# Kernel tuning notes

Hardware: AMD Instinct MI355X
Metric: run time of the kernel (lower is better)

The kernel has to match this reference:

```python
import jax, jax.numpy as jnp
import numpy as np

D_MODEL = 1024
N_HEADS = 16
HEAD_DIM = D_MODEL // N_HEADS  # 64
N_T = max(1, int(N_HEADS * 0.25))  # 4 time heads
N_S = N_HEADS - N_T               # 12 space heads
T_DIM = N_T * HEAD_DIM
S_DIM = N_S * HEAD_DIM
B, L = 2, 2048


def setup_inputs() -> dict:
    key = jax.random.key(0)
    ks = jax.random.split(key, 8)
    std = 0.02
    return {
        "x": jax.random.normal(ks[0], (B, L, D_MODEL), dtype=jnp.float32),
        "attention_mask": jnp.zeros((B, 1, 1, L), dtype=jnp.float32),
        # torch nn.Linear weights have shape (out_features, in_features)
        "w_qt": jax.random.normal(ks[1], (T_DIM, D_MODEL), dtype=jnp.float32) * std,
        "w_kt": jax.random.normal(ks[2], (T_DIM, D_MODEL), dtype=jnp.float32) * std,
        "w_qs": jax.random.normal(ks[3], (S_DIM, D_MODEL), dtype=jnp.float32) * std,
        "w_ks": jax.random.normal(ks[4], (S_DIM, D_MODEL), dtype=jnp.float32) * std,
        "w_sigma": jnp.zeros((1,), dtype=jnp.float32),
        "w_v": jax.random.normal(ks[5], (D_MODEL, D_MODEL), dtype=jnp.float32) * std,
        "w_o": jax.random.normal(ks[6], (D_MODEL, D_MODEL), dtype=jnp.float32) * std,
    }


def _heads(x, w, n_h):
    # x:(B,L,D) @ w.T:(D,out) -> (B,L,n_h,d_h) -> (B,n_h,L,d_h)
    b, l, _ = x.shape
    y = jnp.einsum('bld,td->blt', x, w)
    return y.reshape(b, l, n_h, HEAD_DIM).transpose(0, 2, 1, 3)


def reference(x, attention_mask, w_qt, w_kt, w_qs, w_ks, w_sigma, w_v, w_o):
    b, l, _ = x.shape
    scale = np.sqrt(HEAD_DIM).astype(np.float32)
    # F3: time heads (sign-flipped, scaled by learnable sigma) + space heads
    Qt = _heads(x, w_qt, N_T)
    Kt = _heads(x, w_kt, N_T)
    Qs = _heads(x, w_qs, N_S)
    Ks = _heads(x, w_ks, N_S)
    st = jnp.einsum('bhqd,bhkd->bhqk', Qt, Kt)  # (B,N_T,L,L)
    ss = jnp.einsum('bhqd,bhkd->bhqk', Qs, Ks)  # (B,N_S,L,L)
    sigma = jax.nn.sigmoid(w_sigma[0])
    score = jnp.concatenate([-sigma * st, ss], axis=1) / scale  # (B,H,L,L)
    score = score + attention_mask.astype(score.dtype)
    attn_probs = jax.nn.softmax(score, axis=-1).astype(x.dtype)
    # dropout p=0.0 -> identity
    V = _heads(x, w_v, N_HEADS)  # (B,H,L,d_h)
    out = jnp.einsum('bhqk,bhkd->bhqd', attn_probs, V)
    out = out.transpose(0, 2, 1, 3).reshape(b, l, D_MODEL)
    out = jnp.einsum('bld,od->blo', out, w_o)
    return out, attn_probs
```

## Files before the change

### kernel.cpp

```cpp
#include <hip/hip_runtime.h>

typedef __bf16 bf16x8 __attribute__((ext_vector_type(8)));
typedef float f32x4 __attribute__((ext_vector_type(4)));
typedef float f32x16 __attribute__((ext_vector_type(16)));
typedef short short4v __attribute__((ext_vector_type(4)));
typedef unsigned short ushort8 __attribute__((ext_vector_type(8)));
typedef unsigned int uint4v __attribute__((ext_vector_type(4)));

#define AS1 __attribute__((address_space(1)))
#define AS3 __attribute__((address_space(3)))
#define GLL16(g, l) __builtin_amdgcn_global_load_lds((const AS1 void*)(g), (AS3 void*)(l), 16, 0, 0)
#define MFMA16(a, b, c) __builtin_amdgcn_mfma_f32_16x16x32_bf16((a), (b), (c), 0, 0, 0)
#define MFMA32(a, b, c) __builtin_amdgcn_mfma_f32_32x32x16_bf16((a), (b), (c), 0, 0, 0)
#define WAITVM(N) asm volatile("s_waitcnt vmcnt(" #N ")" ::: "memory")
#define WAITLGKM0 asm volatile("s_waitcnt lgkmcnt(0)" ::: "memory")
#define L2E 1.44269504f

__device__ __forceinline__ unsigned short f2bf(float f) {
  unsigned int u = __builtin_bit_cast(unsigned int, f);
  u = (u + 0x7fffu + ((u >> 16) & 1u)) >> 16;
  return (unsigned short)u;
}

__device__ __forceinline__ unsigned int cvtpk_bf16(float lo, float hi) {
  unsigned int r;
  asm("v_cvt_pk_bf16_f32 %0, %1, %2" : "=v"(r) : "v"(lo), "v"(hi));
  return r;
}

__global__ void convert_kernel(const float* __restrict__ x,
                               const float* __restrict__ w_qt, const float* __restrict__ w_kt,
                               const float* __restrict__ w_qs, const float* __restrict__ w_ks,
                               const float* __restrict__ w_v, const float* __restrict__ w_o,
                               unsigned short* __restrict__ xb, unsigned short* __restrict__ wcat,
                               unsigned short* __restrict__ wob) {
  const int NX = 4096 * 1024, NW = 3072 * 1024, NO = 1024 * 1024;
  int stride = gridDim.x * blockDim.x;
  for (int i = blockIdx.x * blockDim.x + threadIdx.x; i < NX + NW + NO; i += stride) {
    if (i < NX) {
      xb[i] = f2bf(x[i]);
    } else if (i < NX + NW) {
      int j = i - NX;
      int n = j >> 10, k = j & 1023;
      const float* src;
      if (n < 256)        src = w_qt + n * 1024;
      else if (n < 1024)  src = w_qs + (n - 256) * 1024;
      else if (n < 1280)  src = w_kt + (n - 1024) * 1024;
      else if (n < 2048)  src = w_ks + (n - 1280) * 1024;
      else                src = w_v + (n - 2048) * 1024;
      wcat[j] = f2bf(src[k]);
    } else {
      int j = i - NX - NW;
      wob[j] = f2bf(w_o[j]);
    }
  }
}

__global__ __launch_bounds__(256) void gemm_qkv(const unsigned short* __restrict__ A,
                                                const unsigned short* __restrict__ Bw,
                                                const float* __restrict__ amask,
                                                unsigned short* __restrict__ qb,
                                                unsigned short* __restrict__ kb,
                                                unsigned short* __restrict__ vt) {
  __shared__ unsigned short As[128 * 32];
  __shared__ unsigned short Bs[128 * 32];
  const int t = threadIdx.x;
  const int lane = t & 63, wid = t >> 6;
  const int wm = wid >> 1, wn = wid & 1;
  const int lr = lane & 15, lg = lane >> 4;
  const int m0 = blockIdx.x * 128, n0 = blockIdx.y * 128;
  const int K = 1024;
  f32x4 acc[4][4] = {};
  const unsigned short* gA0 = A + (m0 + (t >> 2)) * K + (t & 3) * 8;
  const unsigned short* gB0 = Bw + (n0 + (t >> 2)) * K + (t & 3) * 8;
  char* lA = (char*)As + wid * 1024;
  char* lB = (char*)Bs + wid * 1024;
  for (int k0 = 0; k0 < K; k0 += 32) {
    __syncthreads();
    GLL16(gA0 + k0, lA);
    GLL16(gA0 + 64 * K + k0, lA + 4096);
    GLL16(gB0 + k0, lB);
    GLL16(gB0 + 64 * K + k0, lB + 4096);
    __syncthreads();
    bf16x8 af[4], bfr[4];
#pragma unroll
    for (int i = 0; i < 4; ++i) {
      af[i] = *(const bf16x8*)&As[(wm * 64 + i * 16 + lr) * 32 + lg * 8];
      bfr[i] = *(const bf16x8*)&Bs[(wn * 64 + i * 16 + lr) * 32 + lg * 8];
    }
#pragma unroll
    for (int i = 0; i < 4; ++i)
#pragma unroll
      for (int j = 0; j < 4; ++j)
        acc[i][j] = MFMA16(af[i], bfr[j], acc[i][j]);
  }
#pragma unroll
  for (int i = 0; i < 4; ++i) {
#pragma unroll
    for (int j = 0; j < 4; ++j) {
      int n = n0 + wn * 64 + j * 16 + lr;
      int mb = m0 + wm * 64 + i * 16 + lg * 4;
      f32x4 v = acc[i][j];
      if (n < 2048) {
        unsigned short* dst = (n < 1024) ? qb : kb;
        int nn = n & 1023;
        int h = nn >> 6, d = nn & 63;
#pragma unroll
        for (int r = 0; r < 4; ++r) {
          int m = mb + r;
          int b = m >> 11, l = m & 2047;
          dst[((b * 16 + h) * 2048 + l) * 64 + d] = f2bf(v[r]);
        }
      } else {
        int nn = n - 2048;
        int h = nn >> 6, d = nn & 63;
        int b = mb >> 11, l = mb & 2047;
        const float* mrow = amask + b * 2048 + l;
        short4v pk;
#pragma unroll
        for (int r = 0; r < 4; ++r)
          pk[r] = (short)f2bf(v[r] * __expf(mrow[r]));
        *(short4v*)&vt[((b * 16 + h) * 64 + d) * 2048 + l] = pk;
      }
    }
  }
}

__global__ __launch_bounds__(256, 3) void attn_kernel(const unsigned short* __restrict__ qb,
                                                      const unsigned short* __restrict__ kb,
                                                      const unsigned short* __restrict__ vt,
                                                      const float* __restrict__ mask,
                                                      const float* __restrict__ w_sigma,
                                                      float* __restrict__ probs,
                                                      unsigned short* __restrict__ ao) {
  __shared__ __align__(16) char smem[33408];
  const int t = threadIdx.x;
  const int lane = t & 63, w = t >> 6;
  const int col = lane & 31, hi = lane >> 5;
  const int srow = lane >> 3;
  const int schunk = (lane & 7) ^ (srow & 7);
  const int s = blockIdx.x;
  const int bh = (s & 7) * 4 + ((s >> 3) >> 6);
  const int q0 = ((s >> 3) & 63) * 32;
  const int b = bh >> 4, h = bh & 15;
  const float sigma = 1.0f / (1.0f + __expf(-w_sigma[0]));
  const float fac2 = ((h < 4) ? (-sigma * 0.125f) : 0.125f) * L2E;
  const float* maskb = mask + b * 2048;
  const int kbase = w * 512;

  char* Kl = smem + w * 4096;
  char* Vl = smem + 16384 + w * 4096;
  float (*psum)[32] = (float(*)[32])(smem + 32768);
  float* rsum = (float*)(smem + 33280);
  float* pvacc = (float*)smem;

  const unsigned short* kb_bh = kb + (size_t)bh * 2048 * 64;
  const unsigned short* vt_bh = vt + (size_t)bh * 64 * 2048;

  bf16x8 qf[4];
  {
    const unsigned short* qp = qb + (size_t)(bh * 2048 + q0 + col) * 64 + hi * 8;
#pragma unroll
    for (int m = 0; m < 4; ++m) qf[m] = *(const bf16x8*)(qp + m * 16);
  }

#pragma unroll
  for (int j = 0; j < 4; ++j)
    GLL16(kb_bh + (size_t)(kbase + j * 8 + srow) * 64 + schunk * 8, Kl + j * 1024);
  float rs[16];
#pragma unroll
  for (int r = 0; r < 16; ++r) rs[r] = 0.f;
  for (int c = 0; c < 16; ++c) {
    int kc = kbase + c * 32;
    char* curb = (c & 1) ? Vl : Kl;
    char* nxtb = (c & 1) ? Kl : Vl;
    if (c < 15) {
#pragma unroll
      for (int j = 0; j < 4; ++j)
        GLL16(kb_bh + (size_t)(kc + 32 + j * 8 + srow) * 64 + schunk * 8, nxtb + j * 1024);
      WAITVM(4);
    } else {
      WAITVM(0);
    }
    f32x16 sacc = {};
#pragma unroll
    for (int m = 0; m < 4; ++m) {
      bf16x8 kf = *(const bf16x8*)(curb + col * 128 + (((2 * m + hi) ^ (col & 7)) << 4));
      sacc = MFMA32(qf[m], kf, sacc);
    }
    float mv2 = maskb[kc + col] * L2E;
#pragma unroll
    for (int r = 0; r < 16; ++r) rs[r] += exp2f(sacc[r] * fac2 + mv2);
  }
  WAITLGKM0;
#pragma unroll
  for (int j = 0; j < 4; ++j)
    GLL16(kb_bh + (size_t)(kbase + j * 8 + srow) * 64 + schunk * 8, Kl + j * 1024);
#pragma unroll
  for (int j = 0; j < 4; ++j)
    GLL16(vt_bh + (size_t)(j * 8 + srow + (schunk >> 2) * 32) * 2048 + kbase + (schunk & 3) * 8,
          Vl + j * 1024);
#pragma unroll
  for (int o = 1; o < 32; o <<= 1)
#pragma unroll
    for (int r = 0; r < 16; ++r) rs[r] += __shfl_xor(rs[r], o);
  if (col == 0) {
#pragma unroll
    for (int r = 0; r < 16; ++r) psum[w][(r & 3) + 8 * (r >> 2) + 4 * hi] = rs[r];
  }
  __syncthreads();
  if (t < 32) rsum[t] = -log2f(psum[0][t] + psum[1][t] + psum[2][t] + psum[3][t]);
  __syncthreads();

  float rws_l[16];
#pragma unroll
  for (int r = 0; r < 16; ++r) rws_l[r] = rsum[(r & 3) + 8 * (r >> 2) + 4 * hi];
  const float rws_t = rsum[col];

  f32x16 oacc0 = {}, oacc1 = {};
  float* pp = probs + (size_t)(bh * 2048 + q0) * 2048;
  for (int c = 0; c < 16; ++c) {
    int kc = kbase + c * 32;
    if (c == 0) { WAITVM(4); } else { WAITVM(20); }
    bf16x8 kf[4];
#pragma unroll
    for (int m = 0; m < 4; ++m)
      kf[m] = *(const bf16x8*)(Kl + col * 128 + (((2 * m + hi) ^ (col & 7)) << 4));
    f32x16 sn = {}, st_ = {};
#pragma unroll
    for (int m = 0; m < 4; ++m) {
      sn  = MFMA32(qf[m], kf[m], sn);
      st_ = MFMA32(kf[m], qf[m], st_);
    }
    WAITLGKM0;
    if (c < 15) {
#pragma unroll
      for (int j = 0; j < 4; ++j)
        GLL16(kb_bh + (size_t)(kc + 32 + j * 8 + srow) * 64 + schunk * 8, Kl + j * 1024);
    }
    float mv2 = maskb[kc + col] * L2E;
    float pn[16];
#pragma unroll
    for (int r = 0; r < 16; ++r) pn[r] = exp2f(sn[r] * fac2 + (rws_l[r] + mv2));
    float pt[16];
#pragma unroll
    for (int r = 0; r < 16; ++r) pt[r] = exp2f(fminf(st_[r] * fac2 + rws_t, 60.0f));
    unsigned int A0 = cvtpk_bf16(pt[0], pt[1]),  B0 = cvtpk_bf16(pt[4], pt[5]);
    unsigned int C0 = cvtpk_bf16(pt[2], pt[3]),  D0 = cvtpk_bf16(pt[6], pt[7]);
    unsigned int E0 = cvtpk_bf16(pt[8], pt[9]),  F0 = cvtpk_bf16(pt[12], pt[13]);
    unsigned int G0 = cvtpk_bf16(pt[10], pt[11]), H0 = cvtpk_bf16(pt[14], pt[15]);
    asm("v_permlane32_swap_b32 %0, %1" : "+v"(A0), "+v"(B0));
    asm("v_permlane32_swap_b32 %0, %1" : "+v"(C0), "+v"(D0));
    asm("v_permlane32_swap_b32 %0, %1" : "+v"(E0), "+v"(F0));
    asm("v_permlane32_swap_b32 %0, %1" : "+v"(G0), "+v"(H0));
    uint4v u1; u1[0] = A0; u1[1] = C0; u1[2] = B0; u1[3] = D0;
    uint4v u2; u2[0] = E0; u2[1] = G0; u2[2] = F0; u2[3] = H0;
    bf16x8 frag1 = __builtin_bit_cast(bf16x8, u1);
    bf16x8 frag2 = __builtin_bit_cast(bf16x8, u2);
    if (c == 0) { WAITVM(4); } else if (c < 15) { WAITVM(20); } else { WAITVM(16); }
#pragma unroll
    for (int kh = 0; kh < 2; ++kh) {
      bf16x8 pa = (kh == 0) ? frag1 : frag2;
#pragma unroll
      for (int dh = 0; dh < 2; ++dh) {
        bf16x8 vf = *(const bf16x8*)(Vl + col * 128 + (((dh * 4 + kh * 2 + hi) ^ (col & 7)) << 4));
        if (dh == 0) oacc0 = MFMA32(pa, vf, oacc0);
        else         oacc1 = MFMA32(pa, vf, oacc1);
      }
    }
    WAITLGKM0;
    if (c < 15) {
#pragma unroll
      for (int j = 0; j < 4; ++j)
        GLL16(vt_bh + (size_t)(j * 8 + srow + (schunk >> 2) * 32) * 2048 + kc + 32 + (schunk & 3) * 8,
              Vl + j * 1024);
    }
    float* pr = pp + kc + col;
#pragma unroll
    for (int r = 0; r < 16; ++r) {
      int row = (r & 3) + 8 * (r >> 2) + 4 * hi;
      __builtin_nontemporal_store(pn[r], pr + (size_t)row * 2048);
    }
  }

  __syncthreads();
  for (int i = t; i < 2048; i += 256) pvacc[i] = 0.0f;
  __syncthreads();
#pragma unroll
  for (int r = 0; r < 16; ++r) {
    int row = (r & 3) + 8 * (r >> 2) + 4 * hi;
    atomicAdd(&pvacc[row * 64 + col], oacc0[r]);
    atomicAdd(&pvacc[row * 64 + 32 + col], oacc1[r]);
  }
  __syncthreads();
  {
    int row = t >> 3, c8 = (t & 7) * 8;
    f32x4 v0 = *(const f32x4*)&pvacc[row * 64 + c8];
    f32x4 v1 = *(const f32x4*)&pvacc[row * 64 + c8 + 4];
    ushort8 o;
#pragma unroll
    for (int i = 0; i < 4; ++i) {
      o[i] = f2bf(v0[i]);
      o[i + 4] = f2bf(v1[i]);
    }
    *(ushort8*)&ao[((b * 2048) + q0 + row) * 1024 + h * 64 + c8] = o;
  }
}

__global__ __launch_bounds__(256) void gemm_oproj(const unsigned short* __restrict__ A,
                                                  const unsigned short* __restrict__ Bw,
                                                  float* __restrict__ out) {
  __shared__ unsigned short As[128 * 32];
  __shared__ unsigned short Bs[128 * 32];
  const int t = threadIdx.x;
  const int lane = t & 63, wid = t >> 6;
  const int wm = wid >> 1, wn = wid & 1;
  const int lr = lane & 15, lg = lane >> 4;
  const int m0 = blockIdx.x * 128, n0 = blockIdx.y * 128;
  const int K = 1024;
  f32x4 acc[4][4] = {};
  const unsigned short* gA0 = A + (m0 + (t >> 2)) * K + (t & 3) * 8;
  const unsigned short* gB0 = Bw + (n0 + (t >> 2)) * K + (t & 3) * 8;
  char* lA = (char*)As + wid * 1024;
  char* lB = (char*)Bs + wid * 1024;
  for (int k0 = 0; k0 < K; k0 += 32) {
    __syncthreads();
    GLL16(gA0 + k0, lA);
    GLL16(gA0 + 64 * K + k0, lA + 4096);
    GLL16(gB0 + k0, lB);
    GLL16(gB0 + 64 * K + k0, lB + 4096);
    __syncthreads();
    bf16x8 af[4], bfr[4];
#pragma unroll
    for (int i = 0; i < 4; ++i) {
      af[i] = *(const bf16x8*)&As[(wm * 64 + i * 16 + lr) * 32 + lg * 8];
      bfr[i] = *(const bf16x8*)&Bs[(wn * 64 + i * 16 + lr) * 32 + lg * 8];
    }
#pragma unroll
    for (int i = 0; i < 4; ++i)
#pragma unroll
      for (int j = 0; j < 4; ++j)
        acc[i][j] = MFMA16(af[i], bfr[j], acc[i][j]);
  }
#pragma unroll
  for (int i = 0; i < 4; ++i) {
#pragma unroll
    for (int j = 0; j < 4; ++j) {
      int n = n0 + wn * 64 + j * 16 + lr;
      int mb = m0 + wm * 64 + i * 16 + lg * 4;
#pragma unroll
      for (int r = 0; r < 4; ++r)
        out[(mb + r) * 1024 + n] = acc[i][j][r];
    }
  }
}

extern "C" void kernel_launch(void* const* d_in, const int* in_sizes, int n_in,
                              void* d_out, int out_size, void* d_ws, size_t ws_size,
                              hipStream_t stream) {
  const float* x       = (const float*)d_in[0];
  const float* amask   = (const float*)d_in[1];
  const float* w_qt    = (const float*)d_in[2];
  const float* w_kt    = (const float*)d_in[3];
  const float* w_qs    = (const float*)d_in[4];
  const float* w_ks    = (const float*)d_in[5];
  const float* w_sigma = (const float*)d_in[6];
  const float* w_v     = (const float*)d_in[7];
  const float* w_o     = (const float*)d_in[8];

  char* ws = (char*)d_ws;
  unsigned short* xb   = (unsigned short*)ws;
  unsigned short* wcat = (unsigned short*)(ws + 8388608);
  unsigned short* wob  = (unsigned short*)(ws + 14680064);
  unsigned short* qb   = (unsigned short*)(ws + 16777216);
  unsigned short* kb   = (unsigned short*)(ws + 25165824);
  unsigned short* vt   = (unsigned short*)(ws + 33554432);
  unsigned short* ao   = (unsigned short*)(ws + 41943040);

  float* outp = (float*)d_out;
  float* probs = outp + 4194304;

  convert_kernel<<<2048, 256, 0, stream>>>(x, w_qt, w_kt, w_qs, w_ks, w_v, w_o, xb, wcat, wob);
  gemm_qkv<<<dim3(32, 24), 256, 0, stream>>>(xb, wcat, amask, qb, kb, vt);
  attn_kernel<<<2048, 256, 0, stream>>>(qb, kb, vt, amask, w_sigma, probs, ao);
  gemm_oproj<<<dim3(32, 8), 256, 0, stream>>>(ao, wob, outp);
}
```

Before: 337.2 us.

## Store K and V in MFMA fragment order and load directly to registers

The QKV GEMM epilogue now writes K and V into a pre-swizzled layout that matches the 32x32x16 MFMA operand fragments, one 512-element block per fragment. The attention kernel then loads these fragments straight from global memory into registers with coalesced 16-byte loads. This drops the LDS staging, the async global-to-LDS double buffering and the manual waitcnt handling. In exchange it gives up explicit prefetch overlap and relies on the compiler and cache for latency hiding. The GEMM epilogue also does scattered 2-byte stores for K.

```diff
diff --git a/kernel.cpp b/kernel.cpp
--- a/kernel.cpp
+++ b/kernel.cpp
@@ -12,8 +12,6 @@
 #define GLL16(g, l) __builtin_amdgcn_global_load_lds((const AS1 void*)(g), (AS3 void*)(l), 16, 0, 0)
 #define MFMA16(a, b, c) __builtin_amdgcn_mfma_f32_16x16x32_bf16((a), (b), (c), 0, 0, 0)
 #define MFMA32(a, b, c) __builtin_amdgcn_mfma_f32_32x32x16_bf16((a), (b), (c), 0, 0, 0)
-#define WAITVM(N) asm volatile("s_waitcnt vmcnt(" #N ")" ::: "memory")
-#define WAITLGKM0 asm volatile("s_waitcnt lgkmcnt(0)" ::: "memory")
 #define L2E 1.44269504f
 
 __device__ __forceinline__ unsigned short f2bf(float f) {
@@ -60,8 +58,8 @@
                                                 const unsigned short* __restrict__ Bw,
                                                 const float* __restrict__ amask,
                                                 unsigned short* __restrict__ qb,
-                                                unsigned short* __restrict__ kb,
-                                                unsigned short* __restrict__ vt) {
+                                                unsigned short* __restrict__ kfrag,
+                                                unsigned short* __restrict__ vfrag) {
   __shared__ unsigned short As[128 * 32];
   __shared__ unsigned short Bs[128 * 32];
   const int t = threadIdx.x;
@@ -100,45 +98,57 @@
     for (int j = 0; j < 4; ++j) {
       int n = n0 + wn * 64 + j * 16 + lr;
       int mb = m0 + wm * 64 + i * 16 + lg * 4;
+      int b = mb >> 11, l = mb & 2047;
+      int cg = l >> 5;
       f32x4 v = acc[i][j];
-      if (n < 2048) {
-        unsigned short* dst = (n < 1024) ? qb : kb;
-        int nn = n & 1023;
+      if (n < 1024) {
+        int h = n >> 6, d = n & 63;
+#pragma unroll
+        for (int r = 0; r < 4; ++r)
+          qb[((b * 16 + h) * 2048 + l + r) * 64 + d] = f2bf(v[r]);
+      } else if (n < 2048) {
+        int nn = n - 1024;
         int h = nn >> 6, d = nn & 63;
+        int mfr = d >> 4, hi2 = (d >> 3) & 1, e = d & 7;
 #pragma unroll
         for (int r = 0; r < 4; ++r) {
-          int m = mb + r;
-          int b = m >> 11, l = m & 2047;
-          dst[((b * 16 + h) * 2048 + l) * 64 + d] = f2bf(v[r]);
+          int lr2 = l + r;
+          int cgr = lr2 >> 5, ck = lr2 & 31;
+          size_t idx = ((size_t)((b * 16 + h) * 64 + cgr) * 4 + mfr) * 512 + (hi2 * 32 + ck) * 8 + e;
+          kfrag[idx] = f2bf(v[r]);
         }
       } else {
         int nn = n - 2048;
         int h = nn >> 6, d = nn & 63;
-        int b = mb >> 11, l = mb & 2047;
+        int dh = d >> 5, dcol = d & 31;
+        int kk = l & 31;
+        int kh = kk >> 4, hi2 = (kk >> 3) & 1, i0 = kk & 7;
         const float* mrow = amask + b * 2048 + l;
+        size_t idx = ((size_t)((b * 16 + h) * 64 + (l >> 5)) * 4 + (kh * 2 + dh)) * 512
+                     + (hi2 * 32 + dcol) * 8 + i0;
         short4v pk;
 #pragma unroll
         for (int r = 0; r < 4; ++r)
           pk[r] = (short)f2bf(v[r] * __expf(mrow[r]));
-        *(short4v*)&vt[((b * 16 + h) * 64 + d) * 2048 + l] = pk;
+        *(short4v*)&vfrag[idx] = pk;
       }
     }
   }
 }
 
 __global__ __launch_bounds__(256, 3) void attn_kernel(const unsigned short* __restrict__ qb,
-                                                      const unsigned short* __restrict__ kb,
-                                                      const unsigned short* __restrict__ vt,
+                                                      const unsigned short* __restrict__ kfrag,
+                                                      const unsigned short* __restrict__ vfrag,
                                                       const float* __restrict__ mask,
                                                       const float* __restrict__ w_sigma,
                                                       float* __restrict__ probs,
                                                       unsigned short* __restrict__ ao) {
-  __shared__ __align__(16) char smem[33408];
+  __shared__ __align__(16) float pvacc[2048];
+  __shared__ float psum[4][32];
+  __shared__ float rsum[32];
   const int t = threadIdx.x;
   const int lane = t & 63, w = t >> 6;
   const int col = lane & 31, hi = lane >> 5;
-  const int srow = lane >> 3;
-  const int schunk = (lane & 7) ^ (srow & 7);
   const int s = blockIdx.x;
   const int bh = (s & 7) * 4 + ((s >> 3) >> 6);
   const int q0 = ((s >> 3) & 63) * 32;
@@ -146,16 +156,12 @@
   const float sigma = 1.0f / (1.0f + __expf(-w_sigma[0]));
   const float fac2 = ((h < 4) ? (-sigma * 0.125f) : 0.125f) * L2E;
   const float* maskb = mask + b * 2048;
-  const int kbase = w * 512;
-
-  char* Kl = smem + w * 4096;
-  char* Vl = smem + 16384 + w * 4096;
-  float (*psum)[32] = (float(*)[32])(smem + 32768);
-  float* rsum = (float*)(smem + 33280);
-  float* pvacc = (float*)smem;
-
-  const unsigned short* kb_bh = kb + (size_t)bh * 2048 * 64;
-  const unsigned short* vt_bh = vt + (size_t)bh * 64 * 2048;
+  const int cg0 = w * 16;
+
+  const unsigned short* kfb = kfrag + (size_t)bh * 131072;
+  const unsigned short* vfb = vfrag + (size_t)bh * 131072;
+
+  for (int i = t; i < 2048; i += 256) pvacc[i] = 0.0f;
 
   bf16x8 qf[4];
   {
@@ -164,42 +170,25 @@
     for (int m = 0; m < 4; ++m) qf[m] = *(const bf16x8*)(qp + m * 16);
   }
 
-#pragma unroll
-  for (int j = 0; j < 4; ++j)
-    GLL16(kb_bh + (size_t)(kbase + j * 8 + srow) * 64 + schunk * 8, Kl + j * 1024);
   float rs[16];
 #pragma unroll
   for (int r = 0; r < 16; ++r) rs[r] = 0.f;
   for (int c = 0; c < 16; ++c) {
-    int kc = kbase + c * 32;
-    char* curb = (c & 1) ? Vl : Kl;
-    char* nxtb = (c & 1) ? Kl : Vl;
-    if (c < 15) {
-#pragma unroll
-      for (int j = 0; j < 4; ++j)
-        GLL16(kb_bh + (size_t)(kc + 32 + j * 8 + srow) * 64 + schunk * 8, nxtb + j * 1024);
-      WAITVM(4);
-    } else {
-      WAITVM(0);
-    }
+    int cg = cg0 + c;
+    const unsigned short* kp = kfb + (size_t)cg * 2048 + lane * 8;
+    bf16x8 kf0 = *(const bf16x8*)(kp);
+    bf16x8 kf1 = *(const bf16x8*)(kp + 512);
+    bf16x8 kf2 = *(const bf16x8*)(kp + 1024);
+    bf16x8 kf3 = *(const bf16x8*)(kp + 1536);
+    float mv2 = maskb[cg * 32 + col] * L2E;
     f32x16 sacc = {};
-#pragma unroll
-    for (int m = 0; m < 4; ++m) {
-      bf16x8 kf = *(const bf16x8*)(curb + col * 128 + (((2 * m + hi) ^ (col & 7)) << 4));
-      sacc = MFMA32(qf[m], kf, sacc);
-    }
-    float mv2 = maskb[kc + col] * L2E;
+    sacc = MFMA32(qf[0], kf0, sacc);
+    sacc = MFMA32(qf[1], kf1, sacc);
+    sacc = MFMA32(qf[2], kf2, sacc);
+    sacc = MFMA32(qf[3], kf3, sacc);
 #pragma unroll
     for (int r = 0; r < 16; ++r) rs[r] += exp2f(sacc[r] * fac2 + mv2);
   }
-  WAITLGKM0;
-#pragma unroll
-  for (int j = 0; j < 4; ++j)
-    GLL16(kb_bh + (size_t)(kbase + j * 8 + srow) * 64 + schunk * 8, Kl + j * 1024);
-#pragma unroll
-  for (int j = 0; j < 4; ++j)
-    GLL16(vt_bh + (size_t)(j * 8 + srow + (schunk >> 2) * 32) * 2048 + kbase + (schunk & 3) * 8,
-          Vl + j * 1024);
 #pragma unroll
   for (int o = 1; o < 32; o <<= 1)
 #pragma unroll
@@ -220,34 +209,32 @@
   f32x16 oacc0 = {}, oacc1 = {};
   float* pp = probs + (size_t)(bh * 2048 + q0) * 2048;
   for (int c = 0; c < 16; ++c) {
-    int kc = kbase + c * 32;
-    if (c == 0) { WAITVM(4); } else { WAITVM(20); }
-    bf16x8 kf[4];
-#pragma unroll
-    for (int m = 0; m < 4; ++m)
-      kf[m] = *(const bf16x8*)(Kl + col * 128 + (((2 * m + hi) ^ (col & 7)) << 4));
+    int cg = cg0 + c;
+    const unsigned short* kp = kfb + (size_t)cg * 2048 + lane * 8;
+    const unsigned short* vp = vfb + (size_t)cg * 2048 + lane * 8;
+    bf16x8 kf0 = *(const bf16x8*)(kp);
+    bf16x8 kf1 = *(const bf16x8*)(kp + 512);
+    bf16x8 kf2 = *(const bf16x8*)(kp + 1024);
+    bf16x8 kf3 = *(const bf16x8*)(kp + 1536);
+    bf16x8 vf0 = *(const bf16x8*)(vp);
+    bf16x8 vf1 = *(const bf16x8*)(vp + 512);
+    bf16x8 vf2 = *(const bf16x8*)(vp + 1024);
+    bf16x8 vf3 = *(const bf16x8*)(vp + 1536);
+    float mv2 = maskb[cg * 32 + col] * L2E;
     f32x16 sn = {}, st_ = {};
-#pragma unroll
-    for (int m = 0; m < 4; ++m) {
-      sn  = MFMA32(qf[m], kf[m], sn);
-      st_ = MFMA32(kf[m], qf[m], st_);
-    }
-    WAITLGKM0;
-    if (c < 15) {
-#pragma unroll
-      for (int j = 0; j < 4; ++j)
-        GLL16(kb_bh + (size_t)(kc + 32 + j * 8 + srow) * 64 + schunk * 8, Kl + j * 1024);
-    }
-    float mv2 = maskb[kc + col] * L2E;
+    sn = MFMA32(qf[0], kf0, sn);  st_ = MFMA32(kf0, qf[0], st_);
+    sn = MFMA32(qf[1], kf1, sn);  st_ = MFMA32(kf1, qf[1], st_);
+    sn = MFMA32(qf[2], kf2, sn);  st_ = MFMA32(kf2, qf[2], st_);
+    sn = MFMA32(qf[3], kf3, sn);  st_ = MFMA32(kf3, qf[3], st_);
     float pn[16];
 #pragma unroll
     for (int r = 0; r < 16; ++r) pn[r] = exp2f(sn[r] * fac2 + (rws_l[r] + mv2));
     float pt[16];
 #pragma unroll
     for (int r = 0; r < 16; ++r) pt[r] = exp2f(fminf(st_[r] * fac2 + rws_t, 60.0f));
-    unsigned int A0 = cvtpk_bf16(pt[0], pt[1]),  B0 = cvtpk_bf16(pt[4], pt[5]);
-    unsigned int C0 = cvtpk_bf16(pt[2], pt[3]),  D0 = cvtpk_bf16(pt[6], pt[7]);
-    unsigned int E0 = cvtpk_bf16(pt[8], pt[9]),  F0 = cvtpk_bf16(pt[12], pt[13]);
+    unsigned int A0 = cvtpk_bf16(pt[0], pt[1]),   B0 = cvtpk_bf16(pt[4], pt[5]);
+    unsigned int C0 = cvtpk_bf16(pt[2], pt[3]),   D0 = cvtpk_bf16(pt[6], pt[7]);
+    unsigned int E0 = cvtpk_bf16(pt[8], pt[9]),   F0 = cvtpk_bf16(pt[12], pt[13]);
     unsigned int G0 = cvtpk_bf16(pt[10], pt[11]), H0 = cvtpk_bf16(pt[14], pt[15]);
     asm("v_permlane32_swap_b32 %0, %1" : "+v"(A0), "+v"(B0));
     asm("v_permlane32_swap_b32 %0, %1" : "+v"(C0), "+v"(D0));
@@ -257,25 +244,11 @@
     uint4v u2; u2[0] = E0; u2[1] = G0; u2[2] = F0; u2[3] = H0;
     bf16x8 frag1 = __builtin_bit_cast(bf16x8, u1);
     bf16x8 frag2 = __builtin_bit_cast(bf16x8, u2);
-    if (c == 0) { WAITVM(4); } else if (c < 15) { WAITVM(20); } else { WAITVM(16); }
-#pragma unroll
-    for (int kh = 0; kh < 2; ++kh) {
-      bf16x8 pa = (kh == 0) ? frag1 : frag2;
-#pragma unroll
-      for (int dh = 0; dh < 2; ++dh) {
-        bf16x8 vf = *(const bf16x8*)(Vl + col * 128 + (((dh * 4 + kh * 2 + hi) ^ (col & 7)) << 4));
-        if (dh == 0) oacc0 = MFMA32(pa, vf, oacc0);
-        else         oacc1 = MFMA32(pa, vf, oacc1);
-      }
-    }
-    WAITLGKM0;
-    if (c < 15) {
-#pragma unroll
-      for (int j = 0; j < 4; ++j)
-        GLL16(vt_bh + (size_t)(j * 8 + srow + (schunk >> 2) * 32) * 2048 + kc + 32 + (schunk & 3) * 8,
-              Vl + j * 1024);
-    }
-    float* pr = pp + kc + col;
+    oacc0 = MFMA32(frag1, vf0, oacc0);
+    oacc1 = MFMA32(frag1, vf1, oacc1);
+    oacc0 = MFMA32(frag2, vf2, oacc0);
+    oacc1 = MFMA32(frag2, vf3, oacc1);
+    float* pr = pp + cg * 32 + col;
 #pragma unroll
     for (int r = 0; r < 16; ++r) {
       int row = (r & 3) + 8 * (r >> 2) + 4 * hi;
@@ -283,8 +256,6 @@
     }
   }
 
-  __syncthreads();
-  for (int i = t; i < 2048; i += 256) pvacc[i] = 0.0f;
   __syncthreads();
 #pragma unroll
   for (int r = 0; r < 16; ++r) {
@@ -369,19 +340,19 @@
   const float* w_o     = (const float*)d_in[8];
 
   char* ws = (char*)d_ws;
-  unsigned short* xb   = (unsigned short*)ws;
-  unsigned short* wcat = (unsigned short*)(ws + 8388608);
-  unsigned short* wob  = (unsigned short*)(ws + 14680064);
-  unsigned short* qb   = (unsigned short*)(ws + 16777216);
-  unsigned short* kb   = (unsigned short*)(ws + 25165824);
-  unsigned short* vt   = (unsigned short*)(ws + 33554432);
-  unsigned short* ao   = (unsigned short*)(ws + 41943040);
+  unsigned short* xb    = (unsigned short*)ws;
+  unsigned short* wcat  = (unsigned short*)(ws + 8388608);
+  unsigned short* wob   = (unsigned short*)(ws + 14680064);
+  unsigned short* qb    = (unsigned short*)(ws + 16777216);
+  unsigned short* kfrag = (unsigned short*)(ws + 25165824);
+  unsigned short* vfrag = (unsigned short*)(ws + 33554432);
+  unsigned short* ao    = (unsigned short*)(ws + 41943040);
 
   float* outp = (float*)d_out;
   float* probs = outp + 4194304;
 
   convert_kernel<<<2048, 256, 0, stream>>>(x, w_qt, w_kt, w_qs, w_ks, w_v, w_o, xb, wcat, wob);
-  gemm_qkv<<<dim3(32, 24), 256, 0, stream>>>(xb, wcat, amask, qb, kb, vt);
-  attn_kernel<<<2048, 256, 0, stream>>>(qb, kb, vt, amask, w_sigma, probs, ao);
+  gemm_qkv<<<dim3(32, 24), 256, 0, stream>>>(xb, wcat, amask, qb, kfrag, vfrag);
+  attn_kernel<<<2048, 256, 0, stream>>>(qb, kfrag, vfrag, amask, w_sigma, probs, ao);
   gemm_oproj<<<dim3(32, 8), 256, 0, stream>>>(ao, wob, outp);
 }
```

Result: faster. 273.7 us (-18.8%).
